# Performance work log

Measured on AMD Instinct MI355X. Metric: run time of the kernel, lower is better.

## Reference

```python
import jax, jax.numpy as jnp
import numpy as np

EPS = 1e-6

def _rms_norm(x, w):
    # per-head RMSNorm over last dim (head_dim)
    var = jnp.mean(jnp.square(x), axis=-1, keepdims=True)
    return x * jax.lax.rsqrt(var + EPS) * w

def _linear(x, w, b):
    # torch nn.Linear: y = x @ W^T + b
    return jnp.einsum('bsd,od->bso', x, w) + b

def setup_inputs() -> dict:
    key = jax.random.key(0)
    ks = jax.random.split(key, 16)
    B, S, S_enc, D, H, HD = 1, 2048, 256, 1536, 24, 64
    w = lambda k: jax.random.normal(k, (D, D), dtype=jnp.float32) * 0.02
    return {
        'hidden_states': jax.random.normal(ks[0], (B, S, D), dtype=jnp.float32),
        'encoder_hidden_states': jax.random.normal(ks[1], (B, S_enc, D), dtype=jnp.float32),
        'attention_mask': jnp.zeros((B, 1, 1, S + S_enc), dtype=jnp.float32),
        'to_q_weight': w(ks[2]), 'to_q_bias': jnp.zeros((D,), jnp.float32),
        'to_k_weight': w(ks[3]), 'to_k_bias': jnp.zeros((D,), jnp.float32),
        'to_v_weight': w(ks[4]), 'to_v_bias': jnp.zeros((D,), jnp.float32),
        'norm_q_weight': jnp.ones((HD,), jnp.float32),
        'norm_k_weight': jnp.ones((HD,), jnp.float32),
        'add_q_proj_weight': w(ks[5]), 'add_q_proj_bias': jnp.zeros((D,), jnp.float32),
        'add_k_proj_weight': w(ks[6]), 'add_k_proj_bias': jnp.zeros((D,), jnp.float32),
        'add_v_proj_weight': w(ks[7]), 'add_v_proj_bias': jnp.zeros((D,), jnp.float32),
        'norm_added_q_weight': jnp.ones((HD,), jnp.float32),
        'norm_added_k_weight': jnp.ones((HD,), jnp.float32),
        'to_out_0_weight': w(ks[8]), 'to_out_0_bias': jnp.zeros((D,), jnp.float32),
        'to_add_out_weight': w(ks[9]), 'to_add_out_bias': jnp.zeros((D,), jnp.float32),
        'attn_heads': 24,
        'attn_head_dim': 64,
    }

def reference(hidden_states, encoder_hidden_states, attention_mask,
              to_q_weight, to_q_bias, to_k_weight, to_k_bias, to_v_weight, to_v_bias,
              norm_q_weight, norm_k_weight,
              add_q_proj_weight, add_q_proj_bias, add_k_proj_weight, add_k_proj_bias,
              add_v_proj_weight, add_v_proj_bias,
              norm_added_q_weight, norm_added_k_weight,
              to_out_0_weight, to_out_0_bias, to_add_out_weight, to_add_out_bias,
              attn_heads, attn_head_dim):
    B, S, D = hidden_states.shape
    S_enc = encoder_hidden_states.shape[1]
    H, HD = attn_heads, attn_head_dim
    scale = float(HD) ** -0.5

    def split_heads(x):  # [B,T,H*HD] -> [B,H,T,HD]
        return x.reshape(B, -1, H, HD).transpose(0, 2, 1, 3)

    # hidden-stream QKV + per-head RMSNorm on q,k
    q = _rms_norm(split_heads(_linear(hidden_states, to_q_weight, to_q_bias)), norm_q_weight)
    k = _rms_norm(split_heads(_linear(hidden_states, to_k_weight, to_k_bias)), norm_k_weight)
    v = split_heads(_linear(hidden_states, to_v_weight, to_v_bias))

    # encoder-stream QKV + per-head RMSNorm on q,k
    eq = _rms_norm(split_heads(_linear(encoder_hidden_states, add_q_proj_weight, add_q_proj_bias)), norm_added_q_weight)
    ek = _rms_norm(split_heads(_linear(encoder_hidden_states, add_k_proj_weight, add_k_proj_bias)), norm_added_k_weight)
    ev = split_heads(_linear(encoder_hidden_states, add_v_proj_weight, add_v_proj_bias))

    # concat streams along sequence: [B,H,S+S_enc,HD]
    q = jnp.concatenate([q, eq], axis=2)
    k = jnp.concatenate([k, ek], axis=2)
    v = jnp.concatenate([v, ev], axis=2)

    # SDPA with additive mask
    scores = jnp.einsum('bhqd,bhkd->bhqk', q, k) * scale + attention_mask
    probs = jax.nn.softmax(scores, axis=-1)
    out = jnp.einsum('bhqk,bhkd->bhqd', probs, v)  # [B,H,T,HD]
    out = out.transpose(0, 2, 1, 3).reshape(B, S + S_enc, H * HD)

    # split back into image / text streams, separate output projections
    attn_output = _linear(out[:, :S], to_out_0_weight, to_out_0_bias)
    context_attn_output = _linear(out[:, S:], to_add_out_weight, to_add_out_bias)
    del context_attn_output  # AttentionFunc returns only the hidden-stream output
    return attn_output
```

## Files before the change

### kernel.cpp

```cpp
#include <hip/hip_runtime.h>
#include <cstdint>


typedef __attribute__((ext_vector_type(8))) short s16x8;
typedef __attribute__((ext_vector_type(4))) float f32x4;

#define LOG2E 1.4426950408889634f

__device__ __forceinline__ short f2bf(float f) {
  union { float f; uint32_t u; } v; v.f = f;
  uint32_t r = v.u + 0x7FFFu + ((v.u >> 16) & 1u);
  return (short)(r >> 16);
}
__device__ __forceinline__ short f2bf_fast(float f) {
  union { float f; uint32_t u; } v; v.f = f;
  return (short)((v.u + 0x8000u) >> 16);
}

typedef uint32_t __attribute__((address_space(1)))* gas_u32;
typedef uint32_t __attribute__((address_space(3)))* las_u32;

__device__ __forceinline__ void gload_lds16(const short* g, short* l) {
  __builtin_amdgcn_global_load_lds((gas_u32)(g), (las_u32)(l), 16, 0, 0);
}

struct CvtSeg { const float* src; short* dst; int n4; };
struct CvtArgs { CvtSeg s[8]; };

__global__ __launch_bounds__(256) void cvt_bf16_kernel(CvtArgs a) {
  const int stride = gridDim.x * blockDim.x;
  const int tid = blockIdx.x * blockDim.x + threadIdx.x;
  for (int i = 0; i < 8; ++i) {
    const float4* src = (const float4*)a.s[i].src;
    short* dst = a.s[i].dst;
    const int n4 = a.s[i].n4;
    for (int j = tid; j < n4; j += stride) {
      float4 v = src[j];
      short4 o;
      o.x = f2bf(v.x); o.y = f2bf(v.y); o.z = f2bf(v.z); o.w = f2bf(v.w);
      *(short4*)(dst + (size_t)j * 4) = o;
    }
  }
}

enum { MODE_Q = 0, MODE_K = 1, MODE_V = 2, MODE_OUT = 3 };

struct GemmCfg {
  const short* A;
  const short* W;
  const float* bias;
  const float* normw;
  void* dst;
  int toff;
  int mode;
  int mtiles;
};
struct GemmArgs { GemmCfg c[5]; };

__global__ __launch_bounds__(256) void proj_gemm_kernel(GemmArgs args) {
  const GemmCfg cfg = args.c[blockIdx.z];
  if ((int)blockIdx.y >= cfg.mtiles) return;
  constexpr int K = 1536;
  __shared__ short As[4096];
  __shared__ short Bs[4096];
  const int t = threadIdx.x;
  const int lane = t & 63;
  const int wave = t >> 6;
  const int l16 = lane & 15;
  const int quad = lane >> 4;
  const int wm = wave >> 1;
  const int wn = wave & 1;

  const short* __restrict__ Ag = cfg.A + (size_t)(blockIdx.y * 128) * K;
  const short* __restrict__ Wg = cfg.W + (size_t)(blockIdx.x * 128) * K;
  const int srow = t >> 2;
  const int scol = (t & 3) << 3;

  const f32x4 z4 = {0.f, 0.f, 0.f, 0.f};
  f32x4 acc[4][4];
#pragma unroll
  for (int i = 0; i < 4; ++i) {
#pragma unroll
    for (int j = 0; j < 4; ++j) acc[i][j] = z4;
  }

  for (int k0 = 0; k0 < K; k0 += 32) {
    gload_lds16(Ag + (size_t)srow * K + k0 + scol, As + t * 8);
    gload_lds16(Ag + (size_t)(srow + 64) * K + k0 + scol, As + 2048 + t * 8);
    gload_lds16(Wg + (size_t)srow * K + k0 + scol, Bs + t * 8);
    gload_lds16(Wg + (size_t)(srow + 64) * K + k0 + scol, Bs + 2048 + t * 8);
    __syncthreads();
    s16x8 af[4], bfr[4];
#pragma unroll
    for (int i = 0; i < 4; ++i)
      af[i] = *(const s16x8*)(As + (wm * 64 + i * 16 + l16) * 32 + quad * 8);
#pragma unroll
    for (int i = 0; i < 4; ++i)
      bfr[i] = *(const s16x8*)(Bs + (wn * 64 + i * 16 + l16) * 32 + quad * 8);
#pragma unroll
    for (int mi = 0; mi < 4; ++mi) {
#pragma unroll
      for (int ni = 0; ni < 4; ++ni)
        acc[mi][ni] = __builtin_amdgcn_mfma_f32_16x16x32_bf16(af[mi], bfr[ni], acc[mi][ni], 0, 0, 0);
    }
    __syncthreads();
  }

  const int nbase = blockIdx.x * 128 + wn * 64;
  const int mbase = blockIdx.y * 128 + wm * 64;
  const int mode = cfg.mode;
  const int h = nbase >> 6;

  float biasv[4], nwv[4];
#pragma unroll
  for (int ni = 0; ni < 4; ++ni) {
    int col = nbase + ni * 16 + l16;
    biasv[ni] = cfg.bias[col];
    nwv[ni] = (mode == MODE_Q || mode == MODE_K) ? cfg.normw[col & 63] : 0.f;
  }

#pragma unroll
  for (int mi = 0; mi < 4; ++mi) {
    float vv[4][4];
#pragma unroll
    for (int ni = 0; ni < 4; ++ni) {
#pragma unroll
      for (int r = 0; r < 4; ++r) vv[ni][r] = acc[mi][ni][r] + biasv[ni];
    }
    if (mode == MODE_Q || mode == MODE_K) {
      float ss[4];
#pragma unroll
      for (int r = 0; r < 4; ++r)
        ss[r] = vv[0][r] * vv[0][r] + vv[1][r] * vv[1][r] +
                vv[2][r] * vv[2][r] + vv[3][r] * vv[3][r];
#pragma unroll
      for (int r = 0; r < 4; ++r) {
        ss[r] += __shfl_xor(ss[r], 1);
        ss[r] += __shfl_xor(ss[r], 2);
        ss[r] += __shfl_xor(ss[r], 4);
        ss[r] += __shfl_xor(ss[r], 8);
        float rs = rsqrtf(ss[r] * (1.0f / 64.0f) + 1e-6f);
#pragma unroll
        for (int ni = 0; ni < 4; ++ni) vv[ni][r] *= rs * nwv[ni];
      }
    }
    const int row0 = mbase + mi * 16 + quad * 4;
    if (mode == MODE_Q) {
      short* Qd = (short*)cfg.dst;
#pragma unroll
      for (int ni = 0; ni < 4; ++ni) {
        int d = ni * 16 + l16;
#pragma unroll
        for (int r = 0; r < 4; ++r)
          Qd[((size_t)h * 2048 + row0 + r) * 64 + d] = f2bf(vv[ni][r]);
      }
    } else if (mode == MODE_K) {
      short* Kd = (short*)cfg.dst;
#pragma unroll
      for (int ni = 0; ni < 4; ++ni) {
        int d = ni * 16 + l16;
#pragma unroll
        for (int r = 0; r < 4; ++r)
          Kd[((size_t)h * 2304 + cfg.toff + row0 + r) * 64 + d] = f2bf(vv[ni][r]);
      }
    } else if (mode == MODE_V) {
      short* Vd = (short*)cfg.dst;
#pragma unroll
      for (int ni = 0; ni < 4; ++ni) {
        int d = ni * 16 + l16;
        short4 o4;
        o4.x = f2bf(vv[ni][0]); o4.y = f2bf(vv[ni][1]);
        o4.z = f2bf(vv[ni][2]); o4.w = f2bf(vv[ni][3]);
        *(short4*)(Vd + ((size_t)h * 64 + d) * 2304 + cfg.toff + row0) = o4;
      }
    } else {
      float* Od = (float*)cfg.dst;
#pragma unroll
      for (int ni = 0; ni < 4; ++ni) {
        int col = nbase + ni * 16 + l16;
#pragma unroll
        for (int r = 0; r < 4; ++r)
          Od[(size_t)(row0 + r) * 1536 + col] = vv[ni][r];
      }
    }
  }
}

__global__ __launch_bounds__(256) void flash_kernel(
    const short* __restrict__ Q, const short* __restrict__ Kc,
    const short* __restrict__ VT, const float* __restrict__ mask,
    short* __restrict__ AO) {
  const int b = blockIdx.x;
  const int h = (b & 7) * 3 + ((b >> 3) % 3);
  const int q0 = ((b >> 3) / 3) * 64;
  const int lane = threadIdx.x & 63;
  const int wave = threadIdx.x >> 6;
  const int qw = wave & 1;
  const int ks = wave >> 1;
  const int l16 = lane & 15;
  const int quad = lane >> 4;

  __shared__ __align__(16) short smem[20480];

  const short* Kh = Kc + (size_t)h * 2304 * 64;
  const short* Vh = VT + (size_t)h * 64 * 2304;

  s16x8 aq0[2], aq1[2];
#pragma unroll
  for (int g = 0; g < 2; ++g) {
    const short* Qrow =
        Q + ((size_t)h * 2048 + q0 + qw * 32 + g * 16 + l16) * 64;
    aq0[g] = *(const s16x8*)(Qrow + quad * 8);
    aq1[g] = *(const s16x8*)(Qrow + quad * 8 + 32);
  }

  s16x8 ones;
#pragma unroll
  for (int i = 0; i < 8; ++i) ones[i] = (short)0x3F80;

  const f32x4 z4 = {0.f, 0.f, 0.f, 0.f};
  f32x4 o[2][4];
#pragma unroll
  for (int g = 0; g < 2; ++g)
#pragma unroll
    for (int ni = 0; ni < 4; ++ni) o[g][ni] = z4;
  f32x4 lacc[2] = {z4, z4};
  const float SC = 0.125f * LOG2E;
  const int kbase = ks * 1152;

  auto stage = [&](int it, int buf) {
    const int kb = kbase + it * 32;
    short* kt = smem + (ks * 2 + buf) * 2048;
    short* vt = smem + 8192 + (ks * 2 + buf) * 2048;
#pragma unroll
    for (int c = 0; c < 2; ++c) {
      const int gi = c * 128 + qw * 64 + lane;
      const int trow = gi >> 3, cp = gi & 7;
      gload_lds16(Kh + (size_t)(kb + trow) * 64 + ((cp ^ (trow & 7)) << 3),
                  kt + c * 1024 + qw * 512 + lane * 8);
      const int d = gi >> 2, cpv = gi & 3;
      gload_lds16(Vh + (size_t)d * 2304 + kb + ((cpv ^ ((d >> 1) & 3)) << 3),
                  vt + c * 1024 + qw * 512 + lane * 8);
    }
  };

  stage(0, 0);
  __syncthreads();

  for (int it = 0; it < 36; ++it) {
    const int buf = it & 1;
    if (it < 35) stage(it + 1, buf ^ 1);
    const short* kt = smem + (ks * 2 + buf) * 2048;
    const short* vt = smem + 8192 + (ks * 2 + buf) * 2048;
    const int kb = kbase + it * 32;

    s16x8 bk[2][2];
#pragma unroll
    for (int ni = 0; ni < 2; ++ni) {
      const int tt = ni * 16 + l16;
      const short* kr = kt + tt * 64;
      bk[ni][0] = *(const s16x8*)(kr + ((quad ^ (tt & 7)) << 3));
      bk[ni][1] = *(const s16x8*)(kr + (((quad + 4) ^ (tt & 7)) << 3));
    }
    s16x8 bv[4];
#pragma unroll
    for (int ni = 0; ni < 4; ++ni) {
      const int d = ni * 16 + l16;
      bv[ni] = *(const s16x8*)(vt + d * 32 + ((quad ^ ((d >> 1) & 3)) << 3));
    }
    float mvl[2];
#pragma unroll
    for (int ni = 0; ni < 2; ++ni) mvl[ni] = mask[kb + ni * 16 + l16] * LOG2E;

#pragma unroll
    for (int g = 0; g < 2; ++g) {
      short* Pg = smem + 16384 + wave * 1024 + g * 512;
#pragma unroll
      for (int ni = 0; ni < 2; ++ni) {
        f32x4 s = __builtin_amdgcn_mfma_f32_16x16x32_bf16(aq0[g], bk[ni][0], z4, 0, 0, 0);
        s = __builtin_amdgcn_mfma_f32_16x16x32_bf16(aq1[g], bk[ni][1], s, 0, 0, 0);
        const int tt = ni * 16 + l16;
        const int cc = tt >> 3;
#pragma unroll
        for (int rr = 0; rr < 4; ++rr) {
          float pv = __builtin_amdgcn_exp2f(fmaf(s[rr], SC, mvl[ni]));
          const int prow = quad * 4 + rr;
          Pg[prow * 32 + ((cc ^ ((prow >> 1) & 3)) << 3) + (tt & 7)] = f2bf_fast(pv);
        }
      }
      s16x8 ap = *(const s16x8*)(Pg + l16 * 32 + ((quad ^ ((l16 >> 1) & 3)) << 3));
      lacc[g] = __builtin_amdgcn_mfma_f32_16x16x32_bf16(ap, ones, lacc[g], 0, 0, 0);
#pragma unroll
      for (int ni = 0; ni < 4; ++ni)
        o[g][ni] = __builtin_amdgcn_mfma_f32_16x16x32_bf16(ap, bv[ni], o[g][ni], 0, 0, 0);
    }
    __syncthreads();
  }

  f32x4* R = (f32x4*)smem;
  if (ks == 1) {
    f32x4* Rw = R + (qw * 64 + lane) * 10;
#pragma unroll
    for (int g = 0; g < 2; ++g) {
#pragma unroll
      for (int ni = 0; ni < 4; ++ni) Rw[g * 5 + ni] = o[g][ni];
      Rw[g * 5 + 4] = lacc[g];
    }
  }
  __syncthreads();
  if (ks == 0) {
    const f32x4* Rw = R + (qw * 64 + lane) * 10;
#pragma unroll
    for (int g = 0; g < 2; ++g) {
#pragma unroll
      for (int ni = 0; ni < 4; ++ni) o[g][ni] += Rw[g * 5 + ni];
      f32x4 ls = lacc[g] + Rw[g * 5 + 4];
#pragma unroll
      for (int rr = 0; rr < 4; ++rr) {
        float inv = 1.0f / ls[rr];
        int tq = q0 + qw * 32 + g * 16 + quad * 4 + rr;
#pragma unroll
        for (int ni = 0; ni < 4; ++ni)
          AO[(size_t)tq * 1536 + h * 64 + ni * 16 + l16] = f2bf(o[g][ni][rr] * inv);
      }
    }
  }
}

extern "C" void kernel_launch(void* const* d_in, const int* in_sizes, int n_in,
                              void* d_out, int out_size, void* d_ws, size_t ws_size,
                              hipStream_t stream) {
  (void)in_sizes; (void)n_in; (void)out_size; (void)ws_size;
  const float* hidden = (const float*)d_in[0];
  const float* enc    = (const float*)d_in[1];
  const float* amask  = (const float*)d_in[2];
  const float* wq  = (const float*)d_in[3];  const float* bq  = (const float*)d_in[4];
  const float* wk  = (const float*)d_in[5];  const float* bk  = (const float*)d_in[6];
  const float* wv  = (const float*)d_in[7];  const float* bv  = (const float*)d_in[8];
  const float* nqw = (const float*)d_in[9];  const float* nkw = (const float*)d_in[10];
  const float* wak = (const float*)d_in[13]; const float* bak = (const float*)d_in[14];
  const float* wav = (const float*)d_in[15]; const float* bav = (const float*)d_in[16];
  const float* nakw = (const float*)d_in[18];
  const float* wo  = (const float*)d_in[19]; const float* bo  = (const float*)d_in[20];
  float* out = (float*)d_out;

  char* p = (char*)d_ws;
  auto carve = [&](size_t bytes) { char* r = p; p += (bytes + 255) & ~(size_t)255; return r; };
  short* Xb   = (short*)carve((size_t)2048 * 1536 * 2);
  short* Eb   = (short*)carve((size_t)256 * 1536 * 2);
  short* Wqb  = (short*)carve((size_t)1536 * 1536 * 2);
  short* Wkb  = (short*)carve((size_t)1536 * 1536 * 2);
  short* Wvb  = (short*)carve((size_t)1536 * 1536 * 2);
  short* Wakb = (short*)carve((size_t)1536 * 1536 * 2);
  short* Wavb = (short*)carve((size_t)1536 * 1536 * 2);
  short* Wob  = (short*)carve((size_t)1536 * 1536 * 2);
  short* Qb   = (short*)carve((size_t)24 * 2048 * 64 * 2);
  short* Kb   = (short*)carve((size_t)24 * 2304 * 64 * 2);
  short* VTb  = (short*)carve((size_t)24 * 64 * 2304 * 2);
  short* AOb  = (short*)carve((size_t)2048 * 1536 * 2);

  CvtArgs ca;
  ca.s[0] = {hidden, Xb, 2048 * 1536 / 4};
  ca.s[1] = {enc,    Eb, 256 * 1536 / 4};
  ca.s[2] = {wq,  Wqb,  1536 * 1536 / 4};
  ca.s[3] = {wk,  Wkb,  1536 * 1536 / 4};
  ca.s[4] = {wv,  Wvb,  1536 * 1536 / 4};
  ca.s[5] = {wak, Wakb, 1536 * 1536 / 4};
  ca.s[6] = {wav, Wavb, 1536 * 1536 / 4};
  ca.s[7] = {wo,  Wob,  1536 * 1536 / 4};
  cvt_bf16_kernel<<<dim3(1024), dim3(256), 0, stream>>>(ca);

  GemmArgs g1;
  g1.c[0] = {Xb, Wqb,  bq,  nqw,     (void*)Qb,  0,    MODE_Q, 16};
  g1.c[1] = {Xb, Wkb,  bk,  nkw,     (void*)Kb,  0,    MODE_K, 16};
  g1.c[2] = {Xb, Wvb,  bv,  nullptr, (void*)VTb, 0,    MODE_V, 16};
  g1.c[3] = {Eb, Wakb, bak, nakw,    (void*)Kb,  2048, MODE_K, 2};
  g1.c[4] = {Eb, Wavb, bav, nullptr, (void*)VTb, 2048, MODE_V, 2};
  proj_gemm_kernel<<<dim3(12, 16, 5), dim3(256), 0, stream>>>(g1);

  flash_kernel<<<dim3(768), dim3(256), 0, stream>>>(Qb, Kb, VTb, amask, AOb);

  GemmArgs g3;
  g3.c[0] = {AOb, Wob, bo, nullptr, (void*)out, 0, MODE_OUT, 16};
  proj_gemm_kernel<<<dim3(12, 16, 1), dim3(256), 0, stream>>>(g3);
}
```

Before: 292.5 us.

## Split-K the output projection and rework flash P staging layout

The output projection GEMM is split into two K halves, launched as separate grid slices, and reduced by a new elementwise add kernel. This raises block count to better fill the GPU, at the cost of an extra fp32 partial buffer and an extra memory pass. In the attention kernel, the probability tile is written with packed 4-element stores into a padded layout and read back element-wise. Global load pointers for K/V staging are precomputed and advanced incrementally to cut address arithmetic.

```diff
diff --git a/kernel.cpp b/kernel.cpp
--- a/kernel.cpp
+++ b/kernel.cpp
@@ -43,6 +43,18 @@
   }
 }
 
+__global__ __launch_bounds__(256) void add_kernel(float* __restrict__ out,
+                                                  const float* __restrict__ part,
+                                                  int n4) {
+  const int stride = gridDim.x * blockDim.x;
+  for (int j = blockIdx.x * blockDim.x + threadIdx.x; j < n4; j += stride) {
+    float4 a = ((const float4*)out)[j];
+    float4 b = ((const float4*)part)[j];
+    a.x += b.x; a.y += b.y; a.z += b.z; a.w += b.w;
+    ((float4*)out)[j] = a;
+  }
+}
+
 enum { MODE_Q = 0, MODE_K = 1, MODE_V = 2, MODE_OUT = 3 };
 
 struct GemmCfg {
@@ -54,6 +66,7 @@
   int toff;
   int mode;
   int mtiles;
+  int kbeg, kend;
 };
 struct GemmArgs { GemmCfg c[5]; };
 
@@ -84,7 +97,7 @@
     for (int j = 0; j < 4; ++j) acc[i][j] = z4;
   }
 
-  for (int k0 = 0; k0 < K; k0 += 32) {
+  for (int k0 = cfg.kbeg; k0 < cfg.kend; k0 += 32) {
     gload_lds16(Ag + (size_t)srow * K + k0 + scol, As + t * 8);
     gload_lds16(Ag + (size_t)(srow + 64) * K + k0 + scol, As + 2048 + t * 8);
     gload_lds16(Wg + (size_t)srow * K + k0 + scol, Bs + t * 8);
@@ -115,7 +128,7 @@
 #pragma unroll
   for (int ni = 0; ni < 4; ++ni) {
     int col = nbase + ni * 16 + l16;
-    biasv[ni] = cfg.bias[col];
+    biasv[ni] = cfg.bias ? cfg.bias[col] : 0.f;
     nwv[ni] = (mode == MODE_Q || mode == MODE_K) ? cfg.normw[col & 63] : 0.f;
   }
 
@@ -200,7 +213,7 @@
   const int l16 = lane & 15;
   const int quad = lane >> 4;
 
-  __shared__ __align__(16) short smem[20480];
+  __shared__ __align__(16) short smem[21504];
 
   const short* Kh = Kc + (size_t)h * 2304 * 64;
   const short* Vh = VT + (size_t)h * 64 * 2304;
@@ -228,30 +241,40 @@
   const float SC = 0.125f * LOG2E;
   const int kbase = ks * 1152;
 
-  auto stage = [&](int it, int buf) {
-    const int kb = kbase + it * 32;
-    short* kt = smem + (ks * 2 + buf) * 2048;
-    short* vt = smem + 8192 + (ks * 2 + buf) * 2048;
+  const short* kgp[2];
+  const short* vgp[2];
+#pragma unroll
+  for (int c = 0; c < 2; ++c) {
+    const int gi = c * 128 + qw * 64 + lane;
+    const int trow = gi >> 3, cp = gi & 7;
+    kgp[c] = Kh + (size_t)(kbase + trow) * 64 + ((cp ^ (trow & 7)) << 3);
+    const int d = gi >> 2, cpv = gi & 3;
+    vgp[c] = Vh + (size_t)d * 2304 + kbase + ((cpv ^ ((d >> 1) & 3)) << 3);
+  }
+  short* ktb[2] = {smem + (ks * 2) * 2048, smem + (ks * 2 + 1) * 2048};
+  short* vtb[2] = {smem + 8192 + (ks * 2) * 2048, smem + 8192 + (ks * 2 + 1) * 2048};
+
+  auto stage = [&](int buf) {
 #pragma unroll
     for (int c = 0; c < 2; ++c) {
-      const int gi = c * 128 + qw * 64 + lane;
-      const int trow = gi >> 3, cp = gi & 7;
-      gload_lds16(Kh + (size_t)(kb + trow) * 64 + ((cp ^ (trow & 7)) << 3),
-                  kt + c * 1024 + qw * 512 + lane * 8);
-      const int d = gi >> 2, cpv = gi & 3;
-      gload_lds16(Vh + (size_t)d * 2304 + kb + ((cpv ^ ((d >> 1) & 3)) << 3),
-                  vt + c * 1024 + qw * 512 + lane * 8);
+      gload_lds16(kgp[c], ktb[buf] + c * 1024 + qw * 512 + lane * 8);
+      gload_lds16(vgp[c], vtb[buf] + c * 1024 + qw * 512 + lane * 8);
+      kgp[c] += 32 * 64;
+      vgp[c] += 32;
     }
   };
 
-  stage(0, 0);
+  stage(0);
   __syncthreads();
+
+  short* Pg0 = smem + 16384 + (wave * 2) * 640;
+  short* Pg1 = Pg0 + 640;
 
   for (int it = 0; it < 36; ++it) {
     const int buf = it & 1;
-    if (it < 35) stage(it + 1, buf ^ 1);
-    const short* kt = smem + (ks * 2 + buf) * 2048;
-    const short* vt = smem + 8192 + (ks * 2 + buf) * 2048;
+    if (it < 35) stage(buf ^ 1);
+    const short* kt = ktb[buf];
+    const short* vt = vtb[buf];
     const int kb = kbase + it * 32;
 
     s16x8 bk[2][2];
@@ -274,25 +297,26 @@
 
 #pragma unroll
     for (int g = 0; g < 2; ++g) {
-      short* Pg = smem + 16384 + wave * 1024 + g * 512;
+      short* Pg = g ? Pg1 : Pg0;
 #pragma unroll
       for (int ni = 0; ni < 2; ++ni) {
         f32x4 s = __builtin_amdgcn_mfma_f32_16x16x32_bf16(aq0[g], bk[ni][0], z4, 0, 0, 0);
         s = __builtin_amdgcn_mfma_f32_16x16x32_bf16(aq1[g], bk[ni][1], s, 0, 0, 0);
-        const int tt = ni * 16 + l16;
-        const int cc = tt >> 3;
-#pragma unroll
-        for (int rr = 0; rr < 4; ++rr) {
-          float pv = __builtin_amdgcn_exp2f(fmaf(s[rr], SC, mvl[ni]));
-          const int prow = quad * 4 + rr;
-          Pg[prow * 32 + ((cc ^ ((prow >> 1) & 3)) << 3) + (tt & 7)] = f2bf_fast(pv);
-        }
-      }
-      s16x8 ap = *(const s16x8*)(Pg + l16 * 32 + ((quad ^ ((l16 >> 1) & 3)) << 3));
-      lacc[g] = __builtin_amdgcn_mfma_f32_16x16x32_bf16(ap, ones, lacc[g], 0, 0, 0);
+        short4 pk;
+        pk.x = f2bf_fast(__builtin_amdgcn_exp2f(fmaf(s[0], SC, mvl[ni])));
+        pk.y = f2bf_fast(__builtin_amdgcn_exp2f(fmaf(s[1], SC, mvl[ni])));
+        pk.z = f2bf_fast(__builtin_amdgcn_exp2f(fmaf(s[2], SC, mvl[ni])));
+        pk.w = f2bf_fast(__builtin_amdgcn_exp2f(fmaf(s[3], SC, mvl[ni])));
+        *(short4*)(Pg + (ni * 16 + l16) * 20 + quad * 4) = pk;
+      }
+      const short* pb = Pg + quad * 160 + l16;
+      union { s16x8 v; short e[8]; } ap;
+#pragma unroll
+      for (int j = 0; j < 8; ++j) ap.e[j] = pb[j * 20];
+      lacc[g] = __builtin_amdgcn_mfma_f32_16x16x32_bf16(ap.v, ones, lacc[g], 0, 0, 0);
 #pragma unroll
       for (int ni = 0; ni < 4; ++ni)
-        o[g][ni] = __builtin_amdgcn_mfma_f32_16x16x32_bf16(ap, bv[ni], o[g][ni], 0, 0, 0);
+        o[g][ni] = __builtin_amdgcn_mfma_f32_16x16x32_bf16(ap.v, bv[ni], o[g][ni], 0, 0, 0);
     }
     __syncthreads();
   }
@@ -358,6 +382,7 @@
   short* Kb   = (short*)carve((size_t)24 * 2304 * 64 * 2);
   short* VTb  = (short*)carve((size_t)24 * 64 * 2304 * 2);
   short* AOb  = (short*)carve((size_t)2048 * 1536 * 2);
+  float* Pbuf = (float*)carve((size_t)2048 * 1536 * 4);
 
   CvtArgs ca;
   ca.s[0] = {hidden, Xb, 2048 * 1536 / 4};
@@ -371,16 +396,18 @@
   cvt_bf16_kernel<<<dim3(1024), dim3(256), 0, stream>>>(ca);
 
   GemmArgs g1;
-  g1.c[0] = {Xb, Wqb,  bq,  nqw,     (void*)Qb,  0,    MODE_Q, 16};
-  g1.c[1] = {Xb, Wkb,  bk,  nkw,     (void*)Kb,  0,    MODE_K, 16};
-  g1.c[2] = {Xb, Wvb,  bv,  nullptr, (void*)VTb, 0,    MODE_V, 16};
-  g1.c[3] = {Eb, Wakb, bak, nakw,    (void*)Kb,  2048, MODE_K, 2};
-  g1.c[4] = {Eb, Wavb, bav, nullptr, (void*)VTb, 2048, MODE_V, 2};
+  g1.c[0] = {Xb, Wqb,  bq,  nqw,     (void*)Qb,  0,    MODE_Q, 16, 0, 1536};
+  g1.c[1] = {Xb, Wkb,  bk,  nkw,     (void*)Kb,  0,    MODE_K, 16, 0, 1536};
+  g1.c[2] = {Xb, Wvb,  bv,  nullptr, (void*)VTb, 0,    MODE_V, 16, 0, 1536};
+  g1.c[3] = {Eb, Wakb, bak, nakw,    (void*)Kb,  2048, MODE_K, 2,  0, 1536};
+  g1.c[4] = {Eb, Wavb, bav, nullptr, (void*)VTb, 2048, MODE_V, 2,  0, 1536};
   proj_gemm_kernel<<<dim3(12, 16, 5), dim3(256), 0, stream>>>(g1);
 
   flash_kernel<<<dim3(768), dim3(256), 0, stream>>>(Qb, Kb, VTb, amask, AOb);
 
   GemmArgs g3;
-  g3.c[0] = {AOb, Wob, bo, nullptr, (void*)out, 0, MODE_OUT, 16};
-  proj_gemm_kernel<<<dim3(12, 16, 1), dim3(256), 0, stream>>>(g3);
-}
+  g3.c[0] = {AOb, Wob, bo,      nullptr, (void*)out,  0, MODE_OUT, 16, 0,   768};
+  g3.c[1] = {AOb, Wob, nullptr, nullptr, (void*)Pbuf, 0, MODE_OUT, 16, 768, 1536};
+  proj_gemm_kernel<<<dim3(12, 16, 2), dim3(256), 0, stream>>>(g3);
+  add_kernel<<<dim3(1024), dim3(256), 0, stream>>>(out, Pbuf, 2048 * 1536 / 4);
+}
```

New measurement: 305.8 us. 1.05x slower.
